# Kernel optimization log

Measured on AMD Instinct MI355X. Metric: run time of the kernel, lower is better.

## Reference

```python
import jax, jax.numpy as jnp
import numpy as np

H = 8          # kv heads
D = 128        # head dim
EPS = 1e-6
NEG = -1e9

def rmsnorm(x, w):
    rms = jnp.sqrt(jnp.mean(x * x, axis=-1, keepdims=True) + EPS)
    return x / rms * w

def apply_rotary(x, cos, sin):
    # x: [B, h, T, D]; cos/sin: [1, 1, T, D/2]
    x1, x2 = jnp.split(x, 2, axis=-1)
    return jnp.concatenate([x1 * cos - x2 * sin, x1 * sin + x2 * cos], axis=-1)


def setup_inputs() -> dict:
    key = jax.random.key(0)
    ks = jax.random.split(key, 7)
    B, T, hid = 1, 4096, 1024
    s = 0.02
    return {
        "x":   jax.random.normal(ks[0], (B, T, hid), jnp.float32),
        "cos": jax.random.normal(ks[1], (1, 1, T, D // 2), jnp.float32),
        "sin": jax.random.normal(ks[2], (1, 1, T, D // 2), jnp.float32),
        "Wq":  jax.random.normal(ks[3], (hid, 2 * hid), jnp.float32) * s,
        "Wk":  jax.random.normal(ks[4], (hid, hid), jnp.float32) * s,
        "Wv":  jax.random.normal(ks[5], (hid, hid), jnp.float32) * s,
        "Wo":  jax.random.normal(ks[6], (2 * hid, hid), jnp.float32) * s,
        "qn_w": jnp.ones((D,), jnp.float32),
        "kn_w": jnp.ones((D,), jnp.float32),
    }


def reference(x, cos, sin, Wq, Wk, Wv, Wo, qn_w, kn_w):
    B, T, _ = x.shape
    scale = D ** -0.5

    q = (x @ Wq).reshape(B, T, 2 * H, D).transpose(0, 2, 1, 3)  # [B,2H,T,D]
    k = (x @ Wk).reshape(B, T, H, D).transpose(0, 2, 1, 3)      # [B,H,T,D]
    v = (x @ Wv).reshape(B, T, H, D).transpose(0, 2, 1, 3)      # [B,H,T,D]

    q = apply_rotary(rmsnorm(q, qn_w), cos, sin)
    k = apply_rotary(rmsnorm(k, kn_w), cos, sin)

    # GQA expand: query head i uses kv head i // 2
    k = jnp.repeat(k, 2, axis=1)  # [B,2H,T,D]
    v = jnp.repeat(v, 2, axis=1)

    attn = jnp.einsum("bhtd,bhsd->bhts", q, k) * scale
    causal = jnp.tril(jnp.ones((T, T), bool))
    attn = jnp.where(causal, attn, NEG)
    attn = jax.nn.softmax(attn, axis=-1)

    out = jnp.einsum("bhts,bhsd->bhtd", attn, v)
    out = out.transpose(0, 2, 1, 3).reshape(B, T, 2 * H * D)
    return out @ Wo
```

## Files before the change

kernel.cpp:

```cpp
#include <hip/hip_runtime.h>
#include <hip/hip_bf16.h>

#define H2 16
#define HKV 8
#define DHEAD 128
#define HID 1024
#define NQ 2048

typedef unsigned short u16;
typedef __bf16 bf16x8 __attribute__((ext_vector_type(8)));
typedef float f32x4 __attribute__((ext_vector_type(4)));

__device__ __forceinline__ u16 f2bf(float x) {
    unsigned int u = __float_as_uint(x);
    unsigned int r = (u + 0x7fffu + ((u >> 16) & 1u)) >> 16;
    return (u16)r;
}
__device__ __forceinline__ float bf2f(u16 x) {
    return __uint_as_float(((unsigned int)x) << 16);
}

__device__ __forceinline__ unsigned int pack_bf16(float hi, float lo) {
    unsigned int a = __float_as_uint(hi) + 0x8000u;
    unsigned int b = __float_as_uint(lo) + 0x8000u;
    return __builtin_amdgcn_perm(a, b, 0x07060302u);
}

__device__ __forceinline__ bf16x8 ld_frag(const u16* p) {
    bf16x8 r;
    *reinterpret_cast<uint4*>(&r) = *reinterpret_cast<const uint4*>(p);
    return r;
}

__device__ __forceinline__ void gload_lds16(const u16* g, u16* l) {
    __builtin_amdgcn_global_load_lds((const __attribute__((address_space(1))) void*)g,
                                     (__attribute__((address_space(3))) void*)l, 16, 0, 0);
}

__global__ __launch_bounds__(256) void cast_f32_bf16(const float* __restrict__ in,
                                                     u16* __restrict__ out, int n4) {
    int i = blockIdx.x * 256 + threadIdx.x;
    if (i < n4) {
        float4 v = reinterpret_cast<const float4*>(in)[i];
        ushort4 o;
        o.x = f2bf(v.x); o.y = f2bf(v.y); o.z = f2bf(v.z); o.w = f2bf(v.w);
        reinterpret_cast<ushort4*>(out)[i] = o;
    }
}

__global__ __launch_bounds__(256) void transpose_cast(const float* __restrict__ in,
                                                      u16* __restrict__ out, int K, int N) {
    __shared__ u16 t[32][34];
    int k0 = blockIdx.x * 32, n0 = blockIdx.y * 32;
    for (int c = threadIdx.x; c < 1024; c += 256) {
        int k = c >> 5, n = c & 31;
        t[k][n] = f2bf(in[(size_t)(k0 + k) * N + n0 + n]);
    }
    __syncthreads();
    for (int c = threadIdx.x; c < 1024; c += 256) {
        int n = c >> 5, k = c & 31;
        out[(size_t)(n0 + n) * K + k0 + k] = t[k][n];
    }
}

__global__ __launch_bounds__(256) void transpose_cast2(const float* __restrict__ inA,
                                                       const float* __restrict__ inB,
                                                       u16* __restrict__ outA,
                                                       u16* __restrict__ outB, int K, int N) {
    __shared__ u16 t[32][34];
    const float* in = blockIdx.z ? inB : inA;
    u16* out = blockIdx.z ? outB : outA;
    int k0 = blockIdx.x * 32, n0 = blockIdx.y * 32;
    for (int c = threadIdx.x; c < 1024; c += 256) {
        int k = c >> 5, n = c & 31;
        t[k][n] = f2bf(in[(size_t)(k0 + k) * N + n0 + n]);
    }
    __syncthreads();
    for (int c = threadIdx.x; c < 1024; c += 256) {
        int n = c >> 5, k = c & 31;
        out[(size_t)(n0 + n) * K + k0 + k] = t[k][n];
    }
}

__global__ __launch_bounds__(256) void gemm_bf16(const u16* __restrict__ A,
                                                 const u16* __restrict__ Bt,
                                                 float* __restrict__ C,
                                                 int M, int N, int K) {
    __shared__ u16 As[128 * 32];
    __shared__ u16 Bs[128 * 32];
    int tid = threadIdx.x;
    int lane = tid & 63, wave = tid >> 6;
    int quad = lane >> 4, l15 = lane & 15;
    int wr = wave >> 1, wc = wave & 1;
    int m0 = blockIdx.y * 128, n0 = blockIdx.x * 128;

    f32x4 zero = {0.f, 0.f, 0.f, 0.f};
    f32x4 acc[4][4];
    for (int i = 0; i < 4; i++)
        for (int j = 0; j < 4; j++) acc[i][j] = zero;

    int r0 = 16 * wave + (lane >> 2);
    int r1 = r0 + 64;
    int ks0 = (lane & 3) ^ ((r0 >> 1) & 3);
    int ks1 = (lane & 3) ^ ((r1 >> 1) & 3);
    const u16* ga0 = A + (size_t)(m0 + r0) * K + ks0 * 8;
    const u16* ga1 = A + (size_t)(m0 + r1) * K + ks1 * 8;
    const u16* gb0 = Bt + (size_t)(n0 + r0) * K + ks0 * 8;
    const u16* gb1 = Bt + (size_t)(n0 + r1) * K + ks1 * 8;
    u16* la0 = &As[wave * 512];
    u16* la1 = &As[(wave + 4) * 512];
    u16* lb0 = &Bs[wave * 512];
    u16* lb1 = &Bs[(wave + 4) * 512];

    int swz = (quad ^ ((l15 >> 1) & 3)) * 8;

    for (int k0 = 0; k0 < K; k0 += 32) {
        __syncthreads();
        gload_lds16(ga0 + k0, la0);
        gload_lds16(ga1 + k0, la1);
        gload_lds16(gb0 + k0, lb0);
        gload_lds16(gb1 + k0, lb1);
        __syncthreads();
        bf16x8 a[4], b[4];
        #pragma unroll
        for (int i = 0; i < 4; i++) a[i] = ld_frag(&As[(64 * wr + 16 * i + l15) * 32 + swz]);
        #pragma unroll
        for (int j = 0; j < 4; j++) b[j] = ld_frag(&Bs[(64 * wc + 16 * j + l15) * 32 + swz]);
        #pragma unroll
        for (int i = 0; i < 4; i++)
            #pragma unroll
            for (int j = 0; j < 4; j++)
                acc[i][j] = __builtin_amdgcn_mfma_f32_16x16x32_bf16(a[i], b[j], acc[i][j], 0, 0, 0);
    }
    for (int i = 0; i < 4; i++) {
        int rowb = m0 + 64 * wr + 16 * i + quad * 4;
        for (int j = 0; j < 4; j++) {
            int col = n0 + 64 * wc + 16 * j + l15;
            for (int r = 0; r < 4; r++)
                C[(size_t)(rowb + r) * N + col] = acc[i][j][r];
        }
    }
}

__global__ __launch_bounds__(256) void gemm_bf16_ob(const u16* __restrict__ A,
                                                    const u16* __restrict__ Bt,
                                                    u16* __restrict__ C,
                                                    int M, int N, int K) {
    __shared__ u16 As[128 * 32];
    __shared__ u16 Bs[128 * 32];
    int tid = threadIdx.x;
    int lane = tid & 63, wave = tid >> 6;
    int quad = lane >> 4, l15 = lane & 15;
    int wr = wave >> 1, wc = wave & 1;
    int m0 = blockIdx.y * 128, n0 = blockIdx.x * 128;

    f32x4 zero = {0.f, 0.f, 0.f, 0.f};
    f32x4 acc[4][4];
    for (int i = 0; i < 4; i++)
        for (int j = 0; j < 4; j++) acc[i][j] = zero;

    int r0 = 16 * wave + (lane >> 2);
    int r1 = r0 + 64;
    int ks0 = (lane & 3) ^ ((r0 >> 1) & 3);
    int ks1 = (lane & 3) ^ ((r1 >> 1) & 3);
    const u16* ga0 = A + (size_t)(m0 + r0) * K + ks0 * 8;
    const u16* ga1 = A + (size_t)(m0 + r1) * K + ks1 * 8;
    const u16* gb0 = Bt + (size_t)(n0 + r0) * K + ks0 * 8;
    const u16* gb1 = Bt + (size_t)(n0 + r1) * K + ks1 * 8;
    u16* la0 = &As[wave * 512];
    u16* la1 = &As[(wave + 4) * 512];
    u16* lb0 = &Bs[wave * 512];
    u16* lb1 = &Bs[(wave + 4) * 512];

    int swz = (quad ^ ((l15 >> 1) & 3)) * 8;

    for (int k0 = 0; k0 < K; k0 += 32) {
        __syncthreads();
        gload_lds16(ga0 + k0, la0);
        gload_lds16(ga1 + k0, la1);
        gload_lds16(gb0 + k0, lb0);
        gload_lds16(gb1 + k0, lb1);
        __syncthreads();
        bf16x8 a[4], b[4];
        #pragma unroll
        for (int i = 0; i < 4; i++) a[i] = ld_frag(&As[(64 * wr + 16 * i + l15) * 32 + swz]);
        #pragma unroll
        for (int j = 0; j < 4; j++) b[j] = ld_frag(&Bs[(64 * wc + 16 * j + l15) * 32 + swz]);
        #pragma unroll
        for (int i = 0; i < 4; i++)
            #pragma unroll
            for (int j = 0; j < 4; j++)
                acc[i][j] = __builtin_amdgcn_mfma_f32_16x16x32_bf16(a[i], b[j], acc[i][j], 0, 0, 0);
    }
    for (int i = 0; i < 4; i++) {
        int rowb = m0 + 64 * wr + 16 * i + quad * 4;
        for (int j = 0; j < 4; j++) {
            int col = n0 + 64 * wc + 16 * j + l15;
            for (int r = 0; r < 4; r++)
                C[(size_t)(rowb + r) * N + col] = f2bf(acc[i][j][r]);
        }
    }
}

__global__ __launch_bounds__(256) void gemm_bf16_n64(const u16* __restrict__ A,
                                                     const u16* __restrict__ Bt,
                                                     float* __restrict__ C,
                                                     int M, int N, int K) {
    __shared__ u16 As[128 * 32];
    __shared__ u16 Bs[64 * 32];
    int tid = threadIdx.x;
    int lane = tid & 63, wave = tid >> 6;
    int quad = lane >> 4, l15 = lane & 15;
    int m0 = blockIdx.y * 128, n0 = blockIdx.x * 64;

    f32x4 zero = {0.f, 0.f, 0.f, 0.f};
    f32x4 acc[2][4];
    for (int i = 0; i < 2; i++)
        for (int j = 0; j < 4; j++) acc[i][j] = zero;

    int ra0 = 32 * wave + (lane >> 2);
    int ra1 = ra0 + 16;
    int rb  = 16 * wave + (lane >> 2);
    int ksa0 = (lane & 3) ^ ((ra0 >> 1) & 3);
    int ksa1 = (lane & 3) ^ ((ra1 >> 1) & 3);
    int ksb  = (lane & 3) ^ ((rb >> 1) & 3);
    const u16* ga0 = A + (size_t)(m0 + ra0) * K + ksa0 * 8;
    const u16* ga1 = A + (size_t)(m0 + ra1) * K + ksa1 * 8;
    const u16* gb  = Bt + (size_t)(n0 + rb) * K + ksb * 8;
    u16* la0 = &As[(2 * wave) * 512];
    u16* la1 = &As[(2 * wave + 1) * 512];
    u16* lb  = &Bs[wave * 512];

    int swz = (quad ^ ((l15 >> 1) & 3)) * 8;

    for (int k0 = 0; k0 < K; k0 += 32) {
        __syncthreads();
        gload_lds16(ga0 + k0, la0);
        gload_lds16(ga1 + k0, la1);
        gload_lds16(gb + k0, lb);
        __syncthreads();
        bf16x8 a[2], b[4];
        #pragma unroll
        for (int i = 0; i < 2; i++) a[i] = ld_frag(&As[(32 * wave + 16 * i + l15) * 32 + swz]);
        #pragma unroll
        for (int j = 0; j < 4; j++) b[j] = ld_frag(&Bs[(16 * j + l15) * 32 + swz]);
        #pragma unroll
        for (int i = 0; i < 2; i++)
            #pragma unroll
            for (int j = 0; j < 4; j++)
                acc[i][j] = __builtin_amdgcn_mfma_f32_16x16x32_bf16(a[i], b[j], acc[i][j], 0, 0, 0);
    }
    for (int i = 0; i < 2; i++) {
        int rowb = m0 + 32 * wave + 16 * i + quad * 4;
        for (int j = 0; j < 4; j++) {
            int col = n0 + 16 * j + l15;
            for (int r = 0; r < 4; r++)
                C[(size_t)(rowb + r) * N + col] = acc[i][j][r];
        }
    }
}

__global__ __launch_bounds__(256) void norm_rope_qk(const u16* __restrict__ qkv,
                                                    const float* __restrict__ cosp,
                                                    const float* __restrict__ sinp,
                                                    const float* __restrict__ qnw,
                                                    const float* __restrict__ knw,
                                                    u16* __restrict__ Qb,
                                                    u16* __restrict__ Kb,
                                                    int T, float qscale) {
    int wave = threadIdx.x >> 6, lane = threadIdx.x & 63;
    int wid = blockIdx.x * 4 + wave;
    int t = wid / 24, unit = wid % 24;
    if (t >= T) return;
    bool isq = unit < 16;
    int coloff = isq ? unit * 128 : 2048 + (unit - 16) * 128;
    const float* w = isq ? qnw : knw;
    float outscale = isq ? qscale : 1.0f;
    u16* out = isq ? (Qb + ((size_t)unit * T + t) * 128)
                   : (Kb + ((size_t)(unit - 16) * T + t) * 128);
    const u16* r = qkv + (size_t)t * 4096 + coloff;
    float v1 = bf2f(r[lane]), v2 = bf2f(r[lane + 64]);
    float ss = v1 * v1 + v2 * v2;
    for (int off = 1; off < 64; off <<= 1) ss += __shfl_xor(ss, off);
    float inv = rsqrtf(ss * (1.f / 128.f) + 1e-6f);
    float n1 = v1 * inv * w[lane], n2 = v2 * inv * w[lane + 64];
    float c = cosp[(size_t)t * 64 + lane], s = sinp[(size_t)t * 64 + lane];
    float o1 = (n1 * c - n2 * s) * outscale;
    float o2 = (n1 * s + n2 * c) * outscale;
    out[lane] = f2bf(o1);
    out[lane + 64] = f2bf(o2);
}

__global__ __launch_bounds__(256) void v_transpose(const u16* __restrict__ qkv,
                                                   u16* __restrict__ Vbt, int T) {
    __shared__ u16 tt[128][72];
    int h = blockIdx.y, t0 = blockIdx.x * 64;
    for (int c = threadIdx.x; c < 8192; c += 256) {
        int r = c >> 7, d = c & 127;
        tt[d][r] = qkv[(size_t)(t0 + r) * 4096 + 3072 + h * 128 + d];
    }
    __syncthreads();
    for (int c = threadIdx.x; c < 8192; c += 256) {
        int d = c >> 6, r = c & 63;
        Vbt[((size_t)h * 128 + d) * T + t0 + r] = tt[d][r];
    }
}

__global__ __launch_bounds__(256) void flash_attn(const u16* __restrict__ Qb,
                                                  const u16* __restrict__ Kb,
                                                  const u16* __restrict__ Vbt,
                                                  u16* __restrict__ attn, int T) {
    __shared__ u16 Ks[2][64 * 128];
    __shared__ u16 Vt[2][128 * 64];
    __shared__ u16 Ps[64 * 64];
    int tid = threadIdx.x;
    int lane = tid & 63, wave = tid >> 6;
    int quad = lane >> 4, l15 = lane & 15;
    int swb8 = (l15 & 7) * 8;
    int h = blockIdx.y;
    int j = (int)blockIdx.x;
    int kvh = h >> 1;

    const u16* kbase = Kb + (size_t)kvh * T * 128;
    const u16* vbase = Vbt + (size_t)kvh * 128 * T;

    int krow_ = (lane >> 4);
    int kseg_ = (lane & 15);
    int vrow_ = (lane >> 3);
    int vseg_ = (lane & 7);

    auto stage = [&](int s0, int b) {
        #pragma unroll
        for (int i = 0; i < 4; i++) {
            int ch = wave * 4 + i;
            int r = ch * 4 + krow_;
            int s = kseg_ ^ (r & 7);
            gload_lds16(kbase + (size_t)(s0 + r) * 128 + s * 8, &Ks[b][ch * 512]);
        }
        #pragma unroll
        for (int i = 0; i < 4; i++) {
            int ch = wave * 4 + i;
            int d = ch * 8 + vrow_;
            int s = vseg_ ^ (d & 7);
            gload_lds16(vbase + (size_t)d * T + s0 + s * 8, &Vt[b][ch * 512]);
        }
    };

    bf16x8 onesf;
    #pragma unroll
    for (int i = 0; i < 8; i++) onesf[i] = (__bf16)1.0f;
    f32x4 zero = {0.f, 0.f, 0.f, 0.f};
    const float L2E = 1.44269504f;

    for (int pass = 0; pass < 2; ++pass) {
        int qt = pass == 0 ? (63 - j) : j;
        int q0 = qt * 64;

        bf16x8 qf[4];
        {
            const u16* qp = Qb + ((size_t)h * T + q0 + 16 * wave + l15) * 128 + quad * 8;
            #pragma unroll
            for (int kk = 0; kk < 4; kk++) qf[kk] = ld_frag(qp + kk * 32);
        }

        float m_i = -3.0e38f;
        f32x4 lsum = zero;
        f32x4 o[8];
        for (int dt = 0; dt < 8; dt++) o[dt] = zero;

        int ntiles = qt + 1;
        stage(0, 0);
        __syncthreads();

        for (int it = 0; it < ntiles; ++it) {
            int b = it & 1;
            if (it + 1 < ntiles) stage((it + 1) * 64, 1 - b);
            int s0 = it * 64;

            f32x4 scT[4];
            for (int jt = 0; jt < 4; jt++) scT[jt] = zero;
            #pragma unroll
            for (int kk = 0; kk < 4; kk++)
                #pragma unroll
                for (int jt = 0; jt < 4; jt++) {
                    bf16x8 kfrag = ld_frag(&Ks[b][(jt * 16 + l15) * 128 + ((kk * 32 + quad * 8) ^ swb8)]);
                    scT[jt] = __builtin_amdgcn_mfma_f32_16x16x32_bf16(kfrag, qf[kk], scT[jt], 0, 0, 0);
                }

            if (s0 == q0) {
                int qloc = 16 * wave + l15;
                #pragma unroll
                for (int jt = 0; jt < 4; jt++)
                    for (int r = 0; r < 4; r++)
                        if (jt * 16 + quad * 4 + r > qloc) scT[jt][r] = -1e30f;
            }

            float mt = scT[0][0];
            #pragma unroll
            for (int jt = 0; jt < 4; jt++)
                for (int r = 0; r < 4; r++) mt = fmaxf(mt, scT[jt][r]);
            mt = fmaxf(mt, __shfl_xor(mt, 16));
            mt = fmaxf(mt, __shfl_xor(mt, 32));
            float mnew = fmaxf(m_i, mt);
            float alpha = __expf(m_i - mnew);
            m_i = mnew;
            float mls = mnew * L2E;

            #pragma unroll
            for (int jt = 0; jt < 4; jt++)
                for (int r = 0; r < 4; r++)
                    scT[jt][r] = exp2f(fmaf(scT[jt][r], L2E, -mls));

            {
                int prow = 16 * wave + l15;
                #pragma unroll
                for (int jt = 0; jt < 4; jt++) {
                    int s8 = 2 * jt + (quad >> 1);
                    uint2 wv;
                    wv.x = pack_bf16(scT[jt][1], scT[jt][0]);
                    wv.y = pack_bf16(scT[jt][3], scT[jt][2]);
                    *reinterpret_cast<uint2*>(&Ps[prow * 64 + (s8 ^ (l15 & 7)) * 8 + (quad & 1) * 4]) = wv;
                }
            }

            float av[4];
            #pragma unroll
            for (int r = 0; r < 4; r++) av[r] = __shfl(alpha, quad * 4 + r);
            #pragma unroll
            for (int r = 0; r < 4; r++) lsum[r] *= av[r];
            #pragma unroll
            for (int dt = 0; dt < 8; dt++)
                for (int r = 0; r < 4; r++) o[dt][r] *= av[r];

            asm volatile("s_waitcnt lgkmcnt(0)" ::: "memory");

            #pragma unroll
            for (int kk2 = 0; kk2 < 2; kk2++) {
                bf16x8 pa = ld_frag(&Ps[(16 * wave + l15) * 64 + (((4 * kk2 + quad) ^ (l15 & 7)) * 8)]);
                lsum = __builtin_amdgcn_mfma_f32_16x16x32_bf16(pa, onesf, lsum, 0, 0, 0);
                #pragma unroll
                for (int dt = 0; dt < 8; dt++) {
                    bf16x8 vb = ld_frag(&Vt[b][(dt * 16 + l15) * 64 + ((kk2 * 32 + quad * 8) ^ swb8)]);
                    o[dt] = __builtin_amdgcn_mfma_f32_16x16x32_bf16(pa, vb, o[dt], 0, 0, 0);
                }
            }
            __syncthreads();
        }

        float inv[4];
        for (int r = 0; r < 4; r++) inv[r] = 1.f / lsum[r];
        for (int dt = 0; dt < 8; dt++)
            for (int r = 0; r < 4; r++) {
                int row = q0 + 16 * wave + quad * 4 + r;
                attn[(size_t)row * NQ + h * DHEAD + dt * 16 + l15] = f2bf(o[dt][r] * inv[r]);
            }
    }
}

extern "C" void kernel_launch(void* const* d_in, const int* in_sizes, int n_in,
                              void* d_out, int out_size, void* d_ws, size_t ws_size,
                              hipStream_t stream) {
    const float* x    = (const float*)d_in[0];
    const float* cosp = (const float*)d_in[1];
    const float* sinp = (const float*)d_in[2];
    const float* Wq   = (const float*)d_in[3];
    const float* Wk   = (const float*)d_in[4];
    const float* Wv   = (const float*)d_in[5];
    const float* Wo   = (const float*)d_in[6];
    const float* qnw  = (const float*)d_in[7];
    const float* knw  = (const float*)d_in[8];
    float* out = (float*)d_out;
    const int T = in_sizes[1] / 64;

    char* ws = (char*)d_ws;
    size_t off = 0;
    auto alloc = [&](size_t bytes) {
        char* p = ws + off;
        off += (bytes + 255) & ~(size_t)255;
        return p;
    };
    u16*   xb     = (u16*)alloc((size_t)T * HID * 2);
    u16*   Wqkvb  = (u16*)alloc((size_t)4096 * HID * 2);
    u16*   Wob    = (u16*)alloc((size_t)HID * NQ * 2);
    u16*   qkvb   = (u16*)alloc((size_t)T * 4096 * 2);
    u16*   Qb     = (u16*)alloc((size_t)H2 * T * DHEAD * 2);
    u16*   Kb     = (u16*)alloc((size_t)HKV * T * DHEAD * 2);
    u16*   Vbt    = (u16*)alloc((size_t)HKV * DHEAD * T * 2);
    u16*   attn   = (u16*)alloc((size_t)T * NQ * 2);

    cast_f32_bf16<<<(T * HID / 4 + 255) / 256, 256, 0, stream>>>(x, xb, T * HID / 4);
    transpose_cast<<<dim3(HID / 32, NQ / 32), 256, 0, stream>>>(Wq, Wqkvb, HID, NQ);
    transpose_cast2<<<dim3(HID / 32, HID / 32, 2), 256, 0, stream>>>(
        Wk, Wv, Wqkvb + (size_t)2048 * HID, Wqkvb + (size_t)3072 * HID, HID, HID);
    transpose_cast<<<dim3(NQ / 32, HID / 32), 256, 0, stream>>>(Wo, Wob, NQ, HID);

    gemm_bf16_ob<<<dim3(4096 / 128, T / 128), 256, 0, stream>>>(xb, Wqkvb, qkvb, T, 4096, HID);

    const float scale = 0.08838834764831845f;
    norm_rope_qk<<<T * 24 / 4, 256, 0, stream>>>(qkvb, cosp, sinp, qnw, knw, Qb, Kb, T, scale);
    v_transpose<<<dim3(T / 64, HKV), 256, 0, stream>>>(qkvb, Vbt, T);

    flash_attn<<<dim3(32, H2), 256, 0, stream>>>(Qb, Kb, Vbt, attn, T);

    gemm_bf16_n64<<<dim3(HID / 64, T / 128), 256, 0, stream>>>(attn, Wob, out, T, HID, NQ);
}
```

Before: 364.9 us.

## Merge weight transpose launches, double K-step in GEMMs, skip unit rescale

Merges the three weight transpose-cast launches into one kernel that picks its source by block index, so there is less launch overhead. Both GEMM kernels now load two 32-wide K slices per barrier pair (64 per iteration), which halves the synchronization count and doubles LDS use. In flash attention the rescale of the running output and sum is skipped when every lane's alpha is 1. The duplicated GEMM kernels are folded into one template with a bf16 or f32 output flag.

```diff
diff --git a/kernel.cpp b/kernel.cpp
--- a/kernel.cpp
+++ b/kernel.cpp
@@ -48,10 +48,31 @@
     }
 }
 
-__global__ __launch_bounds__(256) void transpose_cast(const float* __restrict__ in,
-                                                      u16* __restrict__ out, int K, int N) {
+__global__ __launch_bounds__(256) void transpose_cast_all(const float* __restrict__ Wq,
+                                                          const float* __restrict__ Wk,
+                                                          const float* __restrict__ Wv,
+                                                          const float* __restrict__ Wo,
+                                                          u16* __restrict__ Wqkvb,
+                                                          u16* __restrict__ Wob) {
     __shared__ u16 t[32][34];
-    int k0 = blockIdx.x * 32, n0 = blockIdx.y * 32;
+    int bid = blockIdx.x;
+    const float* in; u16* out; int K, N, k0, n0;
+    if (bid < 2048) {
+        in = Wq; out = Wqkvb; K = 1024; N = 2048;
+        k0 = (bid & 31) * 32; n0 = (bid >> 5) * 32;
+    } else if (bid < 3072) {
+        int b = bid - 2048;
+        in = Wk; out = Wqkvb + (size_t)2048 * 1024; K = 1024; N = 1024;
+        k0 = (b & 31) * 32; n0 = (b >> 5) * 32;
+    } else if (bid < 4096) {
+        int b = bid - 3072;
+        in = Wv; out = Wqkvb + (size_t)3072 * 1024; K = 1024; N = 1024;
+        k0 = (b & 31) * 32; n0 = (b >> 5) * 32;
+    } else {
+        int b = bid - 4096;
+        in = Wo; out = Wob; K = 2048; N = 1024;
+        k0 = (b & 63) * 32; n0 = (b >> 6) * 32;
+    }
     for (int c = threadIdx.x; c < 1024; c += 256) {
         int k = c >> 5, n = c & 31;
         t[k][n] = f2bf(in[(size_t)(k0 + k) * N + n0 + n]);
@@ -63,31 +84,13 @@
     }
 }
 
-__global__ __launch_bounds__(256) void transpose_cast2(const float* __restrict__ inA,
-                                                       const float* __restrict__ inB,
-                                                       u16* __restrict__ outA,
-                                                       u16* __restrict__ outB, int K, int N) {
-    __shared__ u16 t[32][34];
-    const float* in = blockIdx.z ? inB : inA;
-    u16* out = blockIdx.z ? outB : outA;
-    int k0 = blockIdx.x * 32, n0 = blockIdx.y * 32;
-    for (int c = threadIdx.x; c < 1024; c += 256) {
-        int k = c >> 5, n = c & 31;
-        t[k][n] = f2bf(in[(size_t)(k0 + k) * N + n0 + n]);
-    }
-    __syncthreads();
-    for (int c = threadIdx.x; c < 1024; c += 256) {
-        int n = c >> 5, k = c & 31;
-        out[(size_t)(n0 + n) * K + k0 + k] = t[k][n];
-    }
-}
-
-__global__ __launch_bounds__(256) void gemm_bf16(const u16* __restrict__ A,
-                                                 const u16* __restrict__ Bt,
-                                                 float* __restrict__ C,
-                                                 int M, int N, int K) {
-    __shared__ u16 As[128 * 32];
-    __shared__ u16 Bs[128 * 32];
+template <bool OUT_BF16>
+__global__ __launch_bounds__(256) void gemm_bf16_t(const u16* __restrict__ A,
+                                                   const u16* __restrict__ Bt,
+                                                   void* __restrict__ Cv,
+                                                   int M, int N, int K) {
+    __shared__ u16 As[2][128 * 32];
+    __shared__ u16 Bs[2][128 * 32];
     int tid = threadIdx.x;
     int lane = tid & 63, wave = tid >> 6;
     int quad = lane >> 4, l15 = lane & 15;
@@ -107,97 +110,43 @@
     const u16* ga1 = A + (size_t)(m0 + r1) * K + ks1 * 8;
     const u16* gb0 = Bt + (size_t)(n0 + r0) * K + ks0 * 8;
     const u16* gb1 = Bt + (size_t)(n0 + r1) * K + ks1 * 8;
-    u16* la0 = &As[wave * 512];
-    u16* la1 = &As[(wave + 4) * 512];
-    u16* lb0 = &Bs[wave * 512];
-    u16* lb1 = &Bs[(wave + 4) * 512];
 
     int swz = (quad ^ ((l15 >> 1) & 3)) * 8;
 
-    for (int k0 = 0; k0 < K; k0 += 32) {
+    for (int k0 = 0; k0 < K; k0 += 64) {
         __syncthreads();
-        gload_lds16(ga0 + k0, la0);
-        gload_lds16(ga1 + k0, la1);
-        gload_lds16(gb0 + k0, lb0);
-        gload_lds16(gb1 + k0, lb1);
+        #pragma unroll
+        for (int s = 0; s < 2; s++) {
+            gload_lds16(ga0 + k0 + s * 32, &As[s][wave * 512]);
+            gload_lds16(ga1 + k0 + s * 32, &As[s][(wave + 4) * 512]);
+            gload_lds16(gb0 + k0 + s * 32, &Bs[s][wave * 512]);
+            gload_lds16(gb1 + k0 + s * 32, &Bs[s][(wave + 4) * 512]);
+        }
         __syncthreads();
-        bf16x8 a[4], b[4];
-        #pragma unroll
-        for (int i = 0; i < 4; i++) a[i] = ld_frag(&As[(64 * wr + 16 * i + l15) * 32 + swz]);
-        #pragma unroll
-        for (int j = 0; j < 4; j++) b[j] = ld_frag(&Bs[(64 * wc + 16 * j + l15) * 32 + swz]);
-        #pragma unroll
-        for (int i = 0; i < 4; i++)
-            #pragma unroll
-            for (int j = 0; j < 4; j++)
-                acc[i][j] = __builtin_amdgcn_mfma_f32_16x16x32_bf16(a[i], b[j], acc[i][j], 0, 0, 0);
+        #pragma unroll
+        for (int s = 0; s < 2; s++) {
+            bf16x8 a[4], b[4];
+            #pragma unroll
+            for (int i = 0; i < 4; i++) a[i] = ld_frag(&As[s][(64 * wr + 16 * i + l15) * 32 + swz]);
+            #pragma unroll
+            for (int j = 0; j < 4; j++) b[j] = ld_frag(&Bs[s][(64 * wc + 16 * j + l15) * 32 + swz]);
+            #pragma unroll
+            for (int i = 0; i < 4; i++)
+                #pragma unroll
+                for (int j = 0; j < 4; j++)
+                    acc[i][j] = __builtin_amdgcn_mfma_f32_16x16x32_bf16(a[i], b[j], acc[i][j], 0, 0, 0);
+        }
     }
     for (int i = 0; i < 4; i++) {
         int rowb = m0 + 64 * wr + 16 * i + quad * 4;
         for (int j = 0; j < 4; j++) {
             int col = n0 + 64 * wc + 16 * j + l15;
-            for (int r = 0; r < 4; r++)
-                C[(size_t)(rowb + r) * N + col] = acc[i][j][r];
-        }
-    }
-}
-
-__global__ __launch_bounds__(256) void gemm_bf16_ob(const u16* __restrict__ A,
-                                                    const u16* __restrict__ Bt,
-                                                    u16* __restrict__ C,
-                                                    int M, int N, int K) {
-    __shared__ u16 As[128 * 32];
-    __shared__ u16 Bs[128 * 32];
-    int tid = threadIdx.x;
-    int lane = tid & 63, wave = tid >> 6;
-    int quad = lane >> 4, l15 = lane & 15;
-    int wr = wave >> 1, wc = wave & 1;
-    int m0 = blockIdx.y * 128, n0 = blockIdx.x * 128;
-
-    f32x4 zero = {0.f, 0.f, 0.f, 0.f};
-    f32x4 acc[4][4];
-    for (int i = 0; i < 4; i++)
-        for (int j = 0; j < 4; j++) acc[i][j] = zero;
-
-    int r0 = 16 * wave + (lane >> 2);
-    int r1 = r0 + 64;
-    int ks0 = (lane & 3) ^ ((r0 >> 1) & 3);
-    int ks1 = (lane & 3) ^ ((r1 >> 1) & 3);
-    const u16* ga0 = A + (size_t)(m0 + r0) * K + ks0 * 8;
-    const u16* ga1 = A + (size_t)(m0 + r1) * K + ks1 * 8;
-    const u16* gb0 = Bt + (size_t)(n0 + r0) * K + ks0 * 8;
-    const u16* gb1 = Bt + (size_t)(n0 + r1) * K + ks1 * 8;
-    u16* la0 = &As[wave * 512];
-    u16* la1 = &As[(wave + 4) * 512];
-    u16* lb0 = &Bs[wave * 512];
-    u16* lb1 = &Bs[(wave + 4) * 512];
-
-    int swz = (quad ^ ((l15 >> 1) & 3)) * 8;
-
-    for (int k0 = 0; k0 < K; k0 += 32) {
-        __syncthreads();
-        gload_lds16(ga0 + k0, la0);
-        gload_lds16(ga1 + k0, la1);
-        gload_lds16(gb0 + k0, lb0);
-        gload_lds16(gb1 + k0, lb1);
-        __syncthreads();
-        bf16x8 a[4], b[4];
-        #pragma unroll
-        for (int i = 0; i < 4; i++) a[i] = ld_frag(&As[(64 * wr + 16 * i + l15) * 32 + swz]);
-        #pragma unroll
-        for (int j = 0; j < 4; j++) b[j] = ld_frag(&Bs[(64 * wc + 16 * j + l15) * 32 + swz]);
-        #pragma unroll
-        for (int i = 0; i < 4; i++)
-            #pragma unroll
-            for (int j = 0; j < 4; j++)
-                acc[i][j] = __builtin_amdgcn_mfma_f32_16x16x32_bf16(a[i], b[j], acc[i][j], 0, 0, 0);
-    }
-    for (int i = 0; i < 4; i++) {
-        int rowb = m0 + 64 * wr + 16 * i + quad * 4;
-        for (int j = 0; j < 4; j++) {
-            int col = n0 + 64 * wc + 16 * j + l15;
-            for (int r = 0; r < 4; r++)
-                C[(size_t)(rowb + r) * N + col] = f2bf(acc[i][j][r]);
+            for (int r = 0; r < 4; r++) {
+                if (OUT_BF16)
+                    ((u16*)Cv)[(size_t)(rowb + r) * N + col] = f2bf(acc[i][j][r]);
+                else
+                    ((float*)Cv)[(size_t)(rowb + r) * N + col] = acc[i][j][r];
+            }
         }
     }
 }
@@ -206,8 +155,8 @@
                                                      const u16* __restrict__ Bt,
                                                      float* __restrict__ C,
                                                      int M, int N, int K) {
-    __shared__ u16 As[128 * 32];
-    __shared__ u16 Bs[64 * 32];
+    __shared__ u16 As[2][128 * 32];
+    __shared__ u16 Bs[2][64 * 32];
     int tid = threadIdx.x;
     int lane = tid & 63, wave = tid >> 6;
     int quad = lane >> 4, l15 = lane & 15;
@@ -227,28 +176,31 @@
     const u16* ga0 = A + (size_t)(m0 + ra0) * K + ksa0 * 8;
     const u16* ga1 = A + (size_t)(m0 + ra1) * K + ksa1 * 8;
     const u16* gb  = Bt + (size_t)(n0 + rb) * K + ksb * 8;
-    u16* la0 = &As[(2 * wave) * 512];
-    u16* la1 = &As[(2 * wave + 1) * 512];
-    u16* lb  = &Bs[wave * 512];
 
     int swz = (quad ^ ((l15 >> 1) & 3)) * 8;
 
-    for (int k0 = 0; k0 < K; k0 += 32) {
+    for (int k0 = 0; k0 < K; k0 += 64) {
         __syncthreads();
-        gload_lds16(ga0 + k0, la0);
-        gload_lds16(ga1 + k0, la1);
-        gload_lds16(gb + k0, lb);
+        #pragma unroll
+        for (int s = 0; s < 2; s++) {
+            gload_lds16(ga0 + k0 + s * 32, &As[s][(2 * wave) * 512]);
+            gload_lds16(ga1 + k0 + s * 32, &As[s][(2 * wave + 1) * 512]);
+            gload_lds16(gb + k0 + s * 32, &Bs[s][wave * 512]);
+        }
         __syncthreads();
-        bf16x8 a[2], b[4];
-        #pragma unroll
-        for (int i = 0; i < 2; i++) a[i] = ld_frag(&As[(32 * wave + 16 * i + l15) * 32 + swz]);
-        #pragma unroll
-        for (int j = 0; j < 4; j++) b[j] = ld_frag(&Bs[(16 * j + l15) * 32 + swz]);
-        #pragma unroll
-        for (int i = 0; i < 2; i++)
-            #pragma unroll
-            for (int j = 0; j < 4; j++)
-                acc[i][j] = __builtin_amdgcn_mfma_f32_16x16x32_bf16(a[i], b[j], acc[i][j], 0, 0, 0);
+        #pragma unroll
+        for (int s = 0; s < 2; s++) {
+            bf16x8 a[2], b[4];
+            #pragma unroll
+            for (int i = 0; i < 2; i++) a[i] = ld_frag(&As[s][(32 * wave + 16 * i + l15) * 32 + swz]);
+            #pragma unroll
+            for (int j = 0; j < 4; j++) b[j] = ld_frag(&Bs[s][(16 * j + l15) * 32 + swz]);
+            #pragma unroll
+            for (int i = 0; i < 2; i++)
+                #pragma unroll
+                for (int j = 0; j < 4; j++)
+                    acc[i][j] = __builtin_amdgcn_mfma_f32_16x16x32_bf16(a[i], b[j], acc[i][j], 0, 0, 0);
+        }
     }
     for (int i = 0; i < 2; i++) {
         int rowb = m0 + 32 * wave + 16 * i + quad * 4;
@@ -423,14 +375,16 @@
                 }
             }
 
-            float av[4];
-            #pragma unroll
-            for (int r = 0; r < 4; r++) av[r] = __shfl(alpha, quad * 4 + r);
-            #pragma unroll
-            for (int r = 0; r < 4; r++) lsum[r] *= av[r];
-            #pragma unroll
-            for (int dt = 0; dt < 8; dt++)
-                for (int r = 0; r < 4; r++) o[dt][r] *= av[r];
+            if (__any(alpha != 1.0f)) {
+                float av[4];
+                #pragma unroll
+                for (int r = 0; r < 4; r++) av[r] = __shfl(alpha, quad * 4 + r);
+                #pragma unroll
+                for (int r = 0; r < 4; r++) lsum[r] *= av[r];
+                #pragma unroll
+                for (int dt = 0; dt < 8; dt++)
+                    for (int r = 0; r < 4; r++) o[dt][r] *= av[r];
+            }
 
             asm volatile("s_waitcnt lgkmcnt(0)" ::: "memory");
 
@@ -489,12 +443,9 @@
     u16*   attn   = (u16*)alloc((size_t)T * NQ * 2);
 
     cast_f32_bf16<<<(T * HID / 4 + 255) / 256, 256, 0, stream>>>(x, xb, T * HID / 4);
-    transpose_cast<<<dim3(HID / 32, NQ / 32), 256, 0, stream>>>(Wq, Wqkvb, HID, NQ);
-    transpose_cast2<<<dim3(HID / 32, HID / 32, 2), 256, 0, stream>>>(
-        Wk, Wv, Wqkvb + (size_t)2048 * HID, Wqkvb + (size_t)3072 * HID, HID, HID);
-    transpose_cast<<<dim3(NQ / 32, HID / 32), 256, 0, stream>>>(Wo, Wob, NQ, HID);
-
-    gemm_bf16_ob<<<dim3(4096 / 128, T / 128), 256, 0, stream>>>(xb, Wqkvb, qkvb, T, 4096, HID);
+    transpose_cast_all<<<6144, 256, 0, stream>>>(Wq, Wk, Wv, Wo, Wqkvb, Wob);
+
+    gemm_bf16_t<true><<<dim3(4096 / 128, T / 128), 256, 0, stream>>>(xb, Wqkvb, qkvb, T, 4096, HID);
 
     const float scale = 0.08838834764831845f;
     norm_rope_qk<<<T * 24 / 4, 256, 0, stream>>>(qkvb, cosp, sinp, qnw, knw, Qb, Kb, T, scale);
```

Result: faster. 342.2 us (-6.2%).
